# Kernel optimization log

Measured on AMD Instinct MI355X. Metric: run time of the kernel, lower is better.

The kernel has to match this reference:

```python
import jax, jax.numpy as jnp
import numpy as np

N_NODES = 50000
N_EDGES = 800000
D_IN = 64
D_HID = 256
D_OUT = 64


def _linear_params(key, d_in, d_out):
    kw, kb = jax.random.split(key)
    lim = 1.0 / np.sqrt(d_in)
    W = jax.random.uniform(kw, (d_out, d_in), jnp.float32, -lim, lim)
    b = jax.random.uniform(kb, (d_out,), jnp.float32, -lim, lim)
    return W, b


def setup_inputs() -> dict:
    key = jax.random.key(0)
    ks = jax.random.split(key, 10)
    x = jax.random.normal(ks[0], (N_NODES, D_IN), jnp.float32)
    edge_index = jax.random.randint(ks[1], (2, N_EDGES), 0, N_NODES, jnp.int64)
    edge_attr = jax.random.normal(ks[2], (N_EDGES, D_IN), jnp.float32)
    W1m, b1m = _linear_params(ks[3], D_IN, D_HID)
    W1e, b1e = _linear_params(ks[4], D_IN, D_HID)
    W1s, b1s = _linear_params(ks[5], D_IN, D_HID)
    W2m, b2m = _linear_params(ks[6], D_HID, D_OUT)
    W2e, b2e = _linear_params(ks[7], D_IN, D_OUT)
    W2s, b2s = _linear_params(ks[8], D_HID, D_OUT)
    return dict(x=x, edge_index=edge_index, edge_attr=edge_attr,
                W1m=W1m, b1m=b1m, W1e=W1e, b1e=b1e, W1s=W1s, b1s=b1s,
                W2m=W2m, b2m=b2m, W2e=W2e, b2e=b2e, W2s=W2s, b2s=b2s)


def _general_conv(x, src, dst, edge_attr, Wm, bm, We, be, Ws, bs):
    # lin_msg on nodes (cheaper than on edges), then gather to source of each edge
    x_msg = x @ Wm.T + bm                      # [N, d_out]
    edge_term = edge_attr @ We.T + be          # [E, d_out]
    msg = x_msg[src] + edge_term               # [E, d_out]
    agg = jax.ops.segment_sum(msg, dst, num_segments=x.shape[0])  # scatter-add
    return agg + (x @ Ws.T + bs)               # skip connection (in != out channels)


def reference(x, edge_index, edge_attr,
              W1m, b1m, W1e, b1e, W1s, b1s,
              W2m, b2m, W2e, b2e, W2s, b2s):
    src, dst = edge_index[0], edge_index[1]
    h = _general_conv(x, src, dst, edge_attr, W1m, b1m, W1e, b1e, W1s, b1s)
    h = jax.nn.relu(h)  # dropout is identity in eval mode
    out = _general_conv(h, src, dst, edge_attr, W2m, b2m, W2e, b2e, W2s, b2s)
    return jax.nn.relu(out)
```

## Files before the change

kernel.cpp:

```cpp
#include <hip/hip_runtime.h>

#define NN 50000
#define NE 800000
#define SLOTS 64

typedef float f32x4 __attribute__((ext_vector_type(4)));
typedef short short8 __attribute__((ext_vector_type(8)));

static __device__ __forceinline__ unsigned short f2bf(float f){
  unsigned u = __builtin_bit_cast(unsigned, f);
  u = (u + 0x7fffu + ((u >> 16) & 1u)) >> 16;
  return (unsigned short)u;
}
static __device__ __forceinline__ float bf2f(unsigned short b){
  return __builtin_bit_cast(float, ((unsigned)b) << 16);
}

__global__ __launch_bounds__(256) void k_prep(
    const float* __restrict__ x,
    const float* __restrict__ W1m, const float* __restrict__ b1m,
    const float* __restrict__ W1e, const float* __restrict__ b1e,
    const float* __restrict__ W1s, const float* __restrict__ b1s,
    const float* __restrict__ W2m, const float* __restrict__ b2m,
    const float* __restrict__ W2e, const float* __restrict__ b2e,
    const float* __restrict__ W2s, const float* __restrict__ b2s,
    int* __restrict__ cnt,
    unsigned short* __restrict__ xb,
    unsigned short* __restrict__ W1c, unsigned short* __restrict__ W2c,
    unsigned short* __restrict__ W2mb,
    float* __restrict__ b1sA, float* __restrict__ b1dA,
    float* __restrict__ b2sA, float* __restrict__ b2dA)
{
  int g = blockIdx.x*256 + threadIdx.x;
  if (g < NN*8){
    const float4* xp = (const float4*)x;
    float4 v0 = xp[(size_t)g*2], v1 = xp[(size_t)g*2+1];
    short8 o;
    o[0]=(short)f2bf(v0.x); o[1]=(short)f2bf(v0.y); o[2]=(short)f2bf(v0.z); o[3]=(short)f2bf(v0.w);
    o[4]=(short)f2bf(v1.x); o[5]=(short)f2bf(v1.y); o[6]=(short)f2bf(v1.z); o[7]=(short)f2bf(v1.w);
    *(short8*)(xb + (size_t)g*8) = o;
  }
  if (g < NN) cnt[g] = 0;
  if (g < 256*192){
    int oc = g/192, k = g%192;
    float w = (k<64)? W1m[oc*64+k] : (k<128)? W1e[oc*64+(k-64)] : W1s[oc*64+(k-128)];
    W1c[g] = f2bf(w);
  }
  if (g < 64*320){
    int oc = g/320, k = g%320;
    float w = (k<64)? W2e[oc*64+k] : W2s[oc*256+(k-64)];
    W2c[g] = f2bf(w);
  }
  if (g < 64*256){
    W2mb[g] = f2bf(W2m[g]);
  }
  if (g < 256){ b1sA[g] = b1s[g]; b1dA[g] = b1m[g] + b1e[g]; }
  if (g < 64) { b2sA[g] = b2s[g]; b2dA[g] = b2m[g] + b2e[g]; }
}

__global__ __launch_bounds__(256) void k_scatter1(const int* __restrict__ ei, int* __restrict__ cnt,
    int2* __restrict__ pairs_pad){
  int e = (blockIdx.x*256 + threadIdx.x)*4;
  if (e + 4 <= NE){
    int4 s = *(const int4*)(ei + e);
    int4 d = *(const int4*)(ei + NE + e);
    int p0 = atomicAdd(&cnt[d.x], 1); if (p0 < SLOTS) pairs_pad[d.x*SLOTS + p0] = make_int2(s.x, e+0);
    int p1 = atomicAdd(&cnt[d.y], 1); if (p1 < SLOTS) pairs_pad[d.y*SLOTS + p1] = make_int2(s.y, e+1);
    int p2 = atomicAdd(&cnt[d.z], 1); if (p2 < SLOTS) pairs_pad[d.z*SLOTS + p2] = make_int2(s.z, e+2);
    int p3 = atomicAdd(&cnt[d.w], 1); if (p3 < SLOTS) pairs_pad[d.w*SLOTS + p3] = make_int2(s.w, e+3);
  } else {
    for (int q=e; q<NE; q++){
      int s = ei[q], d = ei[NE+q];
      int pos = atomicAdd(&cnt[d], 1);
      if (pos < SLOTS) pairs_pad[d*SLOTS + pos] = make_int2(s, q);
    }
  }
}

__global__ __launch_bounds__(256) void k_aggA(const int2* __restrict__ pairs,
    const int* __restrict__ cnt,
    const unsigned short* __restrict__ xb, const float* __restrict__ ea,
    unsigned short* __restrict__ in1){
  int v = blockIdx.x*4 + (threadIdx.x>>6);
  int lane = threadIdx.x & 63;
  int slot = lane >> 4, fg = lane & 15;
  if (v >= NN) return;
  int beg = v*SLOTS;
  int end = beg + min(cnt[v], SLOTS);
  float xs[4] = {0,0,0,0}, es[4] = {0,0,0,0};
  float xt[4] = {0,0,0,0}, et[4] = {0,0,0,0};
  int i = beg + slot;
  for (; i + 12 < end; i += 16){
    int2 p0 = pairs[i],   p1 = pairs[i+4];
    int2 p2 = pairs[i+8], p3 = pairs[i+12];
    ushort4 xv0 = *(const ushort4*)(xb + (size_t)p0.x*64 + fg*4);
    ushort4 xv1 = *(const ushort4*)(xb + (size_t)p1.x*64 + fg*4);
    ushort4 xv2 = *(const ushort4*)(xb + (size_t)p2.x*64 + fg*4);
    ushort4 xv3 = *(const ushort4*)(xb + (size_t)p3.x*64 + fg*4);
    f32x4 ev0 = __builtin_nontemporal_load((const f32x4*)(ea + (size_t)p0.y*64 + fg*4));
    f32x4 ev1 = __builtin_nontemporal_load((const f32x4*)(ea + (size_t)p1.y*64 + fg*4));
    f32x4 ev2 = __builtin_nontemporal_load((const f32x4*)(ea + (size_t)p2.y*64 + fg*4));
    f32x4 ev3 = __builtin_nontemporal_load((const f32x4*)(ea + (size_t)p3.y*64 + fg*4));
    xs[0]+=bf2f(xv0.x); xs[1]+=bf2f(xv0.y); xs[2]+=bf2f(xv0.z); xs[3]+=bf2f(xv0.w);
    xt[0]+=bf2f(xv1.x); xt[1]+=bf2f(xv1.y); xt[2]+=bf2f(xv1.z); xt[3]+=bf2f(xv1.w);
    xs[0]+=bf2f(xv2.x); xs[1]+=bf2f(xv2.y); xs[2]+=bf2f(xv2.z); xs[3]+=bf2f(xv2.w);
    xt[0]+=bf2f(xv3.x); xt[1]+=bf2f(xv3.y); xt[2]+=bf2f(xv3.z); xt[3]+=bf2f(xv3.w);
    es[0]+=ev0[0]; es[1]+=ev0[1]; es[2]+=ev0[2]; es[3]+=ev0[3];
    et[0]+=ev1[0]; et[1]+=ev1[1]; et[2]+=ev1[2]; et[3]+=ev1[3];
    es[0]+=ev2[0]; es[1]+=ev2[1]; es[2]+=ev2[2]; es[3]+=ev2[3];
    et[0]+=ev3[0]; et[1]+=ev3[1]; et[2]+=ev3[2]; et[3]+=ev3[3];
  }
  for (; i < end; i += 4){
    int2 p0 = pairs[i];
    ushort4 xv0 = *(const ushort4*)(xb + (size_t)p0.x*64 + fg*4);
    f32x4  ev0 = __builtin_nontemporal_load((const f32x4*)(ea + (size_t)p0.y*64 + fg*4));
    xs[0]+=bf2f(xv0.x); xs[1]+=bf2f(xv0.y); xs[2]+=bf2f(xv0.z); xs[3]+=bf2f(xv0.w);
    es[0]+=ev0[0]; es[1]+=ev0[1]; es[2]+=ev0[2]; es[3]+=ev0[3];
  }
  #pragma unroll
  for (int k=0;k<4;k++){
    float a = xs[k] + xt[k];
    float b = es[k] + et[k];
    a += __shfl_xor(a, 16, 64); a += __shfl_xor(a, 32, 64);
    b += __shfl_xor(b, 16, 64); b += __shfl_xor(b, 32, 64);
    xs[k] = a; es[k] = b;
  }
  if (slot == 0){
    unsigned short* o = in1 + (size_t)v*128;
    ushort4 ox; ox.x=f2bf(xs[0]); ox.y=f2bf(xs[1]); ox.z=f2bf(xs[2]); ox.w=f2bf(xs[3]);
    ushort4 oe; oe.x=f2bf(es[0]); oe.y=f2bf(es[1]); oe.z=f2bf(es[2]); oe.w=f2bf(es[3]);
    *(ushort4*)(o + fg*4)      = ox;
    *(ushort4*)(o + 64 + fg*4) = oe;
  }
}

__global__ __launch_bounds__(256) void k_mega(
  const unsigned short* __restrict__ in1, const unsigned short* __restrict__ xb,
  const unsigned short* __restrict__ W1c,
  const unsigned short* __restrict__ W2mb, const unsigned short* __restrict__ W2c,
  const float* __restrict__ b1sA, const float* __restrict__ b1dA,
  const float* __restrict__ b2sA, const float* __restrict__ b2dA,
  const int* __restrict__ cnt,
  unsigned short* __restrict__ y2, float* __restrict__ z)
{
  __shared__ char hl[64*256*2];
  const int tid = threadIdx.x;
  const int w = tid >> 6, l = tid & 63;
  const int lrow = l & 15, lgrp = l >> 4;
  const int n0 = blockIdx.x * 64;
  const int c0 = w * 64;

  f32x4 acc[4][4];
  #pragma unroll
  for (int i=0;i<4;i++)
    #pragma unroll
    for (int j=0;j<4;j++) acc[i][j] = (f32x4)0.f;

  #pragma unroll 2
  for (int ks=0; ks<6; ks++){
    short8 a[4], b[4];
    #pragma unroll
    for (int rf=0; rf<4; rf++){
      int row = n0 + rf*16 + lrow; if (row >= NN) row = NN-1;
      if (ks < 4) a[rf] = *(const short8*)(in1 + (size_t)row*128 + ks*32 + lgrp*8);
      else        a[rf] = *(const short8*)(xb  + (size_t)row*64 + (ks-4)*32 + lgrp*8);
    }
    #pragma unroll
    for (int cf=0; cf<4; cf++){
      b[cf] = *(const short8*)(W1c + (c0 + cf*16 + lrow)*192 + ks*32 + lgrp*8);
    }
    #pragma unroll
    for (int rf=0; rf<4; rf++)
      #pragma unroll
      for (int cf=0; cf<4; cf++)
        acc[rf][cf] = __builtin_amdgcn_mfma_f32_16x16x32_bf16(a[rf], b[cf], acc[rf][cf], 0, 0, 0);
  }

  float dg[4][4];
  #pragma unroll
  for (int rf=0; rf<4; rf++)
    #pragma unroll
    for (int r=0; r<4; r++){
      int node = n0 + rf*16 + 4*lgrp + r;
      dg[rf][r] = (node < NN) ? (float)cnt[node] : 0.f;
    }

  #pragma unroll
  for (int cf=0; cf<4; cf++){
    int oc = c0 + cf*16 + lrow;
    float bs = b1sA[oc], bd = b1dA[oc];
    #pragma unroll
    for (int rf=0; rf<4; rf++){
      #pragma unroll
      for (int r=0; r<4; r++){
        int rloc = rf*16 + 4*lgrp + r;
        float val = acc[rf][cf][r] + bs + dg[rf][r]*bd;
        val = fmaxf(val, 0.f);
        int byte = (rloc*512 + oc*2) ^ ((rloc & 7) << 4);
        *(unsigned short*)(hl + byte) = f2bf(val);
      }
    }
  }
  __syncthreads();

  const int oc2 = w*16 + lrow;
  f32x4 ay[4], az[4];
  #pragma unroll
  for (int i=0;i<4;i++){ ay[i] = (f32x4)0.f; az[i] = (f32x4)0.f; }

  #pragma unroll 2
  for (int ks=0; ks<8; ks++){
    short8 a2[4];
    #pragma unroll
    for (int rf=0; rf<4; rf++){
      int rloc = rf*16 + lrow;
      int byte = (rloc*512 + (ks*32 + lgrp*8)*2) ^ ((rloc & 7) << 4);
      a2[rf] = *(const short8*)(hl + byte);
    }
    short8 by = *(const short8*)(W2mb + oc2*256 + ks*32 + lgrp*8);
    short8 bz = *(const short8*)(W2c  + oc2*320 + 64 + ks*32 + lgrp*8);
    #pragma unroll
    for (int rf=0; rf<4; rf++){
      ay[rf] = __builtin_amdgcn_mfma_f32_16x16x32_bf16(a2[rf], by, ay[rf], 0, 0, 0);
      az[rf] = __builtin_amdgcn_mfma_f32_16x16x32_bf16(a2[rf], bz, az[rf], 0, 0, 0);
    }
  }
  #pragma unroll
  for (int ks=0; ks<2; ks++){
    short8 a3[4];
    #pragma unroll
    for (int rf=0; rf<4; rf++){
      int row = n0 + rf*16 + lrow; if (row >= NN) row = NN-1;
      a3[rf] = *(const short8*)(in1 + (size_t)row*128 + 64 + ks*32 + lgrp*8);
    }
    short8 be = *(const short8*)(W2c + oc2*320 + ks*32 + lgrp*8);
    #pragma unroll
    for (int rf=0; rf<4; rf++)
      az[rf] = __builtin_amdgcn_mfma_f32_16x16x32_bf16(a3[rf], be, az[rf], 0, 0, 0);
  }

  float bs2 = b2sA[oc2], bd2 = b2dA[oc2];
  #pragma unroll
  for (int rf=0; rf<4; rf++){
    #pragma unroll
    for (int r=0; r<4; r++){
      int node = n0 + rf*16 + 4*lgrp + r;
      if (node < NN){
        y2[(size_t)node*64 + oc2] = f2bf(ay[rf][r]);
        z[(size_t)node*64 + oc2]  = az[rf][r] + bs2 + dg[rf][r]*bd2;
      }
    }
  }
}

__global__ __launch_bounds__(256) void k_aggC(const int2* __restrict__ pairs, const int* __restrict__ cnt,
    const unsigned short* __restrict__ y2, const float* __restrict__ z, float* __restrict__ out){
  int v = blockIdx.x*4 + (threadIdx.x>>6);
  int lane = threadIdx.x & 63;
  int slot = lane >> 4, fg = lane & 15;
  if (v >= NN) return;
  int beg = v*SLOTS;
  int end = beg + min(cnt[v], SLOTS);
  float a[4] = {0,0,0,0}, b[4] = {0,0,0,0};
  int i = beg + slot;
  for (; i + 12 < end; i += 16){
    int s0 = pairs[i].x, s1 = pairs[i+4].x, s2 = pairs[i+8].x, s3 = pairs[i+12].x;
    ushort4 y0 = *(const ushort4*)(y2 + (size_t)s0*64 + fg*4);
    ushort4 y1 = *(const ushort4*)(y2 + (size_t)s1*64 + fg*4);
    ushort4 y2v = *(const ushort4*)(y2 + (size_t)s2*64 + fg*4);
    ushort4 y3 = *(const ushort4*)(y2 + (size_t)s3*64 + fg*4);
    a[0]+=bf2f(y0.x); a[1]+=bf2f(y0.y); a[2]+=bf2f(y0.z); a[3]+=bf2f(y0.w);
    b[0]+=bf2f(y1.x); b[1]+=bf2f(y1.y); b[2]+=bf2f(y1.z); b[3]+=bf2f(y1.w);
    a[0]+=bf2f(y2v.x); a[1]+=bf2f(y2v.y); a[2]+=bf2f(y2v.z); a[3]+=bf2f(y2v.w);
    b[0]+=bf2f(y3.x); b[1]+=bf2f(y3.y); b[2]+=bf2f(y3.z); b[3]+=bf2f(y3.w);
  }
  for (; i < end; i += 4){
    int s0 = pairs[i].x;
    ushort4 y0 = *(const ushort4*)(y2 + (size_t)s0*64 + fg*4);
    a[0]+=bf2f(y0.x); a[1]+=bf2f(y0.y); a[2]+=bf2f(y0.z); a[3]+=bf2f(y0.w);
  }
  #pragma unroll
  for (int k=0;k<4;k++){
    float t = a[k] + b[k];
    t += __shfl_xor(t, 16, 64); t += __shfl_xor(t, 32, 64);
    a[k] = t;
  }
  if (slot == 0){
    const float4 zv = *(const float4*)(z + (size_t)v*64 + fg*4);
    f32x4 o;
    o[0] = fmaxf(zv.x + a[0], 0.f);
    o[1] = fmaxf(zv.y + a[1], 0.f);
    o[2] = fmaxf(zv.z + a[2], 0.f);
    o[3] = fmaxf(zv.w + a[3], 0.f);
    __builtin_nontemporal_store(o, (f32x4*)(out + (size_t)v*64 + fg*4));
  }
}

extern "C" void kernel_launch(void* const* d_in, const int* in_sizes, int n_in,
                              void* d_out, int out_size, void* d_ws, size_t ws_size,
                              hipStream_t stream){
  const float* x   = (const float*)d_in[0];
  const int*   ei  = (const int*)d_in[1];
  const float* ea  = (const float*)d_in[2];
  const float* W1m = (const float*)d_in[3];  const float* b1m = (const float*)d_in[4];
  const float* W1e = (const float*)d_in[5];  const float* b1e = (const float*)d_in[6];
  const float* W1s = (const float*)d_in[7];  const float* b1s = (const float*)d_in[8];
  const float* W2m = (const float*)d_in[9];  const float* b2m = (const float*)d_in[10];
  const float* W2e = (const float*)d_in[11]; const float* b2e = (const float*)d_in[12];
  const float* W2s = (const float*)d_in[13]; const float* b2s = (const float*)d_in[14];
  float* out = (float*)d_out;

  char* base = (char*)d_ws;
  size_t off = 0;
  auto alloc = [&](size_t bytes)->void* {
    void* r = base + off;
    off += (bytes + 255) & ~(size_t)255;
    return r;
  };
  int*   cnt       = (int*)  alloc((size_t)NN*4);
  int2*  pairs_pad = (int2*) alloc(((size_t)NN*SLOTS + SLOTS)*8);
  unsigned short* in1 = (unsigned short*)alloc((size_t)NN*128*2);
  unsigned short* y2  = (unsigned short*)alloc((size_t)NN*64*2);
  float*          z   = (float*)         alloc((size_t)NN*64*4);
  unsigned short* xb  = (unsigned short*)alloc((size_t)NN*64*2);
  unsigned short* W1c = (unsigned short*)alloc((size_t)256*192*2);
  unsigned short* W2c = (unsigned short*)alloc((size_t)64*320*2);
  unsigned short* W2mb= (unsigned short*)alloc((size_t)64*256*2);
  float* b1sA = (float*)alloc(256*4);
  float* b1dA = (float*)alloc(256*4);
  float* b2sA = (float*)alloc(64*4);
  float* b2dA = (float*)alloc(64*4);

  k_prep    <<<(NN*8+255)/256, 256, 0, stream>>>(x, W1m,b1m,W1e,b1e,W1s,b1s,
                                               W2m,b2m,W2e,b2e,W2s,b2s,
                                               cnt, xb, W1c, W2c, W2mb,
                                               b1sA,b1dA,b2sA,b2dA);
  k_scatter1<<<(NE/4+255)/256, 256, 0, stream>>>(ei, cnt, pairs_pad);
  k_aggA    <<<(NN+3)/4, 256, 0, stream>>>(pairs_pad, cnt, xb, ea, in1);
  k_mega    <<<(NN+63)/64, 256, 0, stream>>>(in1, xb, W1c, W2mb, W2c,
                                             b1sA, b1dA, b2sA, b2dA, cnt, y2, z);
  k_aggC    <<<(NN+3)/4, 256, 0, stream>>>(pairs_pad, cnt, y2, z, out);
}
```

Before: 186.0 us.

## Split edge pair buffer into SoA arrays and widen aggC gathers to 16 bytes

Replaces the interleaved (src, edge id) int2 buffer with two separate int arrays, so the second aggregation reads only the source indices it needs instead of discarding half of each 8-byte record. k_aggC now uses 8 lanes per neighbour with 16-byte bf16 loads, giving 8 neighbour slots per wavefront and one more shuffle stage in the reduction. The scatter kernel handles 8 edges per thread, and aggA issues its edge-attribute loads before the node-feature gathers. The scatter now does two separate stores per edge instead of one 8-byte store.

```diff
diff --git a/kernel.cpp b/kernel.cpp
--- a/kernel.cpp
+++ b/kernel.cpp
@@ -59,25 +59,32 @@
 }
 
 __global__ __launch_bounds__(256) void k_scatter1(const int* __restrict__ ei, int* __restrict__ cnt,
-    int2* __restrict__ pairs_pad){
-  int e = (blockIdx.x*256 + threadIdx.x)*4;
-  if (e + 4 <= NE){
-    int4 s = *(const int4*)(ei + e);
-    int4 d = *(const int4*)(ei + NE + e);
-    int p0 = atomicAdd(&cnt[d.x], 1); if (p0 < SLOTS) pairs_pad[d.x*SLOTS + p0] = make_int2(s.x, e+0);
-    int p1 = atomicAdd(&cnt[d.y], 1); if (p1 < SLOTS) pairs_pad[d.y*SLOTS + p1] = make_int2(s.y, e+1);
-    int p2 = atomicAdd(&cnt[d.z], 1); if (p2 < SLOTS) pairs_pad[d.z*SLOTS + p2] = make_int2(s.z, e+2);
-    int p3 = atomicAdd(&cnt[d.w], 1); if (p3 < SLOTS) pairs_pad[d.w*SLOTS + p3] = make_int2(s.w, e+3);
+    int* __restrict__ srcs_pad, int* __restrict__ eids_pad){
+  int e = (blockIdx.x*256 + threadIdx.x)*8;
+  if (e + 8 <= NE){
+    int4 s0 = *(const int4*)(ei + e);
+    int4 s1 = *(const int4*)(ei + e + 4);
+    int4 d0 = *(const int4*)(ei + NE + e);
+    int4 d1 = *(const int4*)(ei + NE + e + 4);
+    int p;
+    p = atomicAdd(&cnt[d0.x], 1); if (p < SLOTS){ srcs_pad[d0.x*SLOTS+p]=s0.x; eids_pad[d0.x*SLOTS+p]=e+0; }
+    p = atomicAdd(&cnt[d0.y], 1); if (p < SLOTS){ srcs_pad[d0.y*SLOTS+p]=s0.y; eids_pad[d0.y*SLOTS+p]=e+1; }
+    p = atomicAdd(&cnt[d0.z], 1); if (p < SLOTS){ srcs_pad[d0.z*SLOTS+p]=s0.z; eids_pad[d0.z*SLOTS+p]=e+2; }
+    p = atomicAdd(&cnt[d0.w], 1); if (p < SLOTS){ srcs_pad[d0.w*SLOTS+p]=s0.w; eids_pad[d0.w*SLOTS+p]=e+3; }
+    p = atomicAdd(&cnt[d1.x], 1); if (p < SLOTS){ srcs_pad[d1.x*SLOTS+p]=s1.x; eids_pad[d1.x*SLOTS+p]=e+4; }
+    p = atomicAdd(&cnt[d1.y], 1); if (p < SLOTS){ srcs_pad[d1.y*SLOTS+p]=s1.y; eids_pad[d1.y*SLOTS+p]=e+5; }
+    p = atomicAdd(&cnt[d1.z], 1); if (p < SLOTS){ srcs_pad[d1.z*SLOTS+p]=s1.z; eids_pad[d1.z*SLOTS+p]=e+6; }
+    p = atomicAdd(&cnt[d1.w], 1); if (p < SLOTS){ srcs_pad[d1.w*SLOTS+p]=s1.w; eids_pad[d1.w*SLOTS+p]=e+7; }
   } else {
     for (int q=e; q<NE; q++){
       int s = ei[q], d = ei[NE+q];
       int pos = atomicAdd(&cnt[d], 1);
-      if (pos < SLOTS) pairs_pad[d*SLOTS + pos] = make_int2(s, q);
-    }
-  }
-}
-
-__global__ __launch_bounds__(256) void k_aggA(const int2* __restrict__ pairs,
+      if (pos < SLOTS){ srcs_pad[d*SLOTS+pos] = s; eids_pad[d*SLOTS+pos] = q; }
+    }
+  }
+}
+
+__global__ __launch_bounds__(256) void k_aggA(const int* __restrict__ srcs, const int* __restrict__ eids,
     const int* __restrict__ cnt,
     const unsigned short* __restrict__ xb, const float* __restrict__ ea,
     unsigned short* __restrict__ in1){
@@ -91,31 +98,31 @@
   float xt[4] = {0,0,0,0}, et[4] = {0,0,0,0};
   int i = beg + slot;
   for (; i + 12 < end; i += 16){
-    int2 p0 = pairs[i],   p1 = pairs[i+4];
-    int2 p2 = pairs[i+8], p3 = pairs[i+12];
-    ushort4 xv0 = *(const ushort4*)(xb + (size_t)p0.x*64 + fg*4);
-    ushort4 xv1 = *(const ushort4*)(xb + (size_t)p1.x*64 + fg*4);
-    ushort4 xv2 = *(const ushort4*)(xb + (size_t)p2.x*64 + fg*4);
-    ushort4 xv3 = *(const ushort4*)(xb + (size_t)p3.x*64 + fg*4);
-    f32x4 ev0 = __builtin_nontemporal_load((const f32x4*)(ea + (size_t)p0.y*64 + fg*4));
-    f32x4 ev1 = __builtin_nontemporal_load((const f32x4*)(ea + (size_t)p1.y*64 + fg*4));
-    f32x4 ev2 = __builtin_nontemporal_load((const f32x4*)(ea + (size_t)p2.y*64 + fg*4));
-    f32x4 ev3 = __builtin_nontemporal_load((const f32x4*)(ea + (size_t)p3.y*64 + fg*4));
+    int q0=eids[i], q1=eids[i+4], q2=eids[i+8], q3=eids[i+12];
+    int s0=srcs[i], s1=srcs[i+4], s2=srcs[i+8], s3=srcs[i+12];
+    f32x4 ev0 = __builtin_nontemporal_load((const f32x4*)(ea + (size_t)q0*64 + fg*4));
+    f32x4 ev1 = __builtin_nontemporal_load((const f32x4*)(ea + (size_t)q1*64 + fg*4));
+    f32x4 ev2 = __builtin_nontemporal_load((const f32x4*)(ea + (size_t)q2*64 + fg*4));
+    f32x4 ev3 = __builtin_nontemporal_load((const f32x4*)(ea + (size_t)q3*64 + fg*4));
+    ushort4 xv0 = *(const ushort4*)(xb + (size_t)s0*64 + fg*4);
+    ushort4 xv1 = *(const ushort4*)(xb + (size_t)s1*64 + fg*4);
+    ushort4 xv2 = *(const ushort4*)(xb + (size_t)s2*64 + fg*4);
+    ushort4 xv3 = *(const ushort4*)(xb + (size_t)s3*64 + fg*4);
+    es[0]+=ev0[0]; es[1]+=ev0[1]; es[2]+=ev0[2]; es[3]+=ev0[3];
+    et[0]+=ev1[0]; et[1]+=ev1[1]; et[2]+=ev1[2]; et[3]+=ev1[3];
+    es[0]+=ev2[0]; es[1]+=ev2[1]; es[2]+=ev2[2]; es[3]+=ev2[3];
+    et[0]+=ev3[0]; et[1]+=ev3[1]; et[2]+=ev3[2]; et[3]+=ev3[3];
     xs[0]+=bf2f(xv0.x); xs[1]+=bf2f(xv0.y); xs[2]+=bf2f(xv0.z); xs[3]+=bf2f(xv0.w);
     xt[0]+=bf2f(xv1.x); xt[1]+=bf2f(xv1.y); xt[2]+=bf2f(xv1.z); xt[3]+=bf2f(xv1.w);
     xs[0]+=bf2f(xv2.x); xs[1]+=bf2f(xv2.y); xs[2]+=bf2f(xv2.z); xs[3]+=bf2f(xv2.w);
     xt[0]+=bf2f(xv3.x); xt[1]+=bf2f(xv3.y); xt[2]+=bf2f(xv3.z); xt[3]+=bf2f(xv3.w);
+  }
+  for (; i < end; i += 4){
+    int q0 = eids[i], s0 = srcs[i];
+    f32x4  ev0 = __builtin_nontemporal_load((const f32x4*)(ea + (size_t)q0*64 + fg*4));
+    ushort4 xv0 = *(const ushort4*)(xb + (size_t)s0*64 + fg*4);
     es[0]+=ev0[0]; es[1]+=ev0[1]; es[2]+=ev0[2]; es[3]+=ev0[3];
-    et[0]+=ev1[0]; et[1]+=ev1[1]; et[2]+=ev1[2]; et[3]+=ev1[3];
-    es[0]+=ev2[0]; es[1]+=ev2[1]; es[2]+=ev2[2]; es[3]+=ev2[3];
-    et[0]+=ev3[0]; et[1]+=ev3[1]; et[2]+=ev3[2]; et[3]+=ev3[3];
-  }
-  for (; i < end; i += 4){
-    int2 p0 = pairs[i];
-    ushort4 xv0 = *(const ushort4*)(xb + (size_t)p0.x*64 + fg*4);
-    f32x4  ev0 = __builtin_nontemporal_load((const f32x4*)(ea + (size_t)p0.y*64 + fg*4));
     xs[0]+=bf2f(xv0.x); xs[1]+=bf2f(xv0.y); xs[2]+=bf2f(xv0.z); xs[3]+=bf2f(xv0.w);
-    es[0]+=ev0[0]; es[1]+=ev0[1]; es[2]+=ev0[2]; es[3]+=ev0[3];
   }
   #pragma unroll
   for (int k=0;k<4;k++){
@@ -253,46 +260,45 @@
   }
 }
 
-__global__ __launch_bounds__(256) void k_aggC(const int2* __restrict__ pairs, const int* __restrict__ cnt,
+__global__ __launch_bounds__(256) void k_aggC(const int* __restrict__ srcs, const int* __restrict__ cnt,
     const unsigned short* __restrict__ y2, const float* __restrict__ z, float* __restrict__ out){
   int v = blockIdx.x*4 + (threadIdx.x>>6);
   int lane = threadIdx.x & 63;
-  int slot = lane >> 4, fg = lane & 15;
+  int slot = lane >> 3, fg = lane & 7;
   if (v >= NN) return;
   int beg = v*SLOTS;
   int end = beg + min(cnt[v], SLOTS);
-  float a[4] = {0,0,0,0}, b[4] = {0,0,0,0};
+  float a[8] = {0,0,0,0,0,0,0,0}, b[8] = {0,0,0,0,0,0,0,0};
   int i = beg + slot;
-  for (; i + 12 < end; i += 16){
-    int s0 = pairs[i].x, s1 = pairs[i+4].x, s2 = pairs[i+8].x, s3 = pairs[i+12].x;
-    ushort4 y0 = *(const ushort4*)(y2 + (size_t)s0*64 + fg*4);
-    ushort4 y1 = *(const ushort4*)(y2 + (size_t)s1*64 + fg*4);
-    ushort4 y2v = *(const ushort4*)(y2 + (size_t)s2*64 + fg*4);
-    ushort4 y3 = *(const ushort4*)(y2 + (size_t)s3*64 + fg*4);
-    a[0]+=bf2f(y0.x); a[1]+=bf2f(y0.y); a[2]+=bf2f(y0.z); a[3]+=bf2f(y0.w);
-    b[0]+=bf2f(y1.x); b[1]+=bf2f(y1.y); b[2]+=bf2f(y1.z); b[3]+=bf2f(y1.w);
-    a[0]+=bf2f(y2v.x); a[1]+=bf2f(y2v.y); a[2]+=bf2f(y2v.z); a[3]+=bf2f(y2v.w);
-    b[0]+=bf2f(y3.x); b[1]+=bf2f(y3.y); b[2]+=bf2f(y3.z); b[3]+=bf2f(y3.w);
-  }
-  for (; i < end; i += 4){
-    int s0 = pairs[i].x;
-    ushort4 y0 = *(const ushort4*)(y2 + (size_t)s0*64 + fg*4);
-    a[0]+=bf2f(y0.x); a[1]+=bf2f(y0.y); a[2]+=bf2f(y0.z); a[3]+=bf2f(y0.w);
-  }
-  #pragma unroll
-  for (int k=0;k<4;k++){
+  for (; i + 8 < end; i += 16){
+    int s0 = srcs[i], s1 = srcs[i+8];
+    short8 y0 = *(const short8*)(y2 + (size_t)s0*64 + fg*8);
+    short8 y1 = *(const short8*)(y2 + (size_t)s1*64 + fg*8);
+    #pragma unroll
+    for (int k=0;k<8;k++){ a[k]+=bf2f((unsigned short)y0[k]); b[k]+=bf2f((unsigned short)y1[k]); }
+  }
+  for (; i < end; i += 8){
+    int s0 = srcs[i];
+    short8 y0 = *(const short8*)(y2 + (size_t)s0*64 + fg*8);
+    #pragma unroll
+    for (int k=0;k<8;k++) a[k]+=bf2f((unsigned short)y0[k]);
+  }
+  #pragma unroll
+  for (int k=0;k<8;k++){
     float t = a[k] + b[k];
-    t += __shfl_xor(t, 16, 64); t += __shfl_xor(t, 32, 64);
+    t += __shfl_xor(t, 8, 64); t += __shfl_xor(t, 16, 64); t += __shfl_xor(t, 32, 64);
     a[k] = t;
   }
   if (slot == 0){
-    const float4 zv = *(const float4*)(z + (size_t)v*64 + fg*4);
-    f32x4 o;
-    o[0] = fmaxf(zv.x + a[0], 0.f);
-    o[1] = fmaxf(zv.y + a[1], 0.f);
-    o[2] = fmaxf(zv.z + a[2], 0.f);
-    o[3] = fmaxf(zv.w + a[3], 0.f);
-    __builtin_nontemporal_store(o, (f32x4*)(out + (size_t)v*64 + fg*4));
+    const float4 z0 = *(const float4*)(z + (size_t)v*64 + fg*8);
+    const float4 z1 = *(const float4*)(z + (size_t)v*64 + fg*8 + 4);
+    f32x4 o0, o1;
+    o0[0] = fmaxf(z0.x + a[0], 0.f); o0[1] = fmaxf(z0.y + a[1], 0.f);
+    o0[2] = fmaxf(z0.z + a[2], 0.f); o0[3] = fmaxf(z0.w + a[3], 0.f);
+    o1[0] = fmaxf(z1.x + a[4], 0.f); o1[1] = fmaxf(z1.y + a[5], 0.f);
+    o1[2] = fmaxf(z1.z + a[6], 0.f); o1[3] = fmaxf(z1.w + a[7], 0.f);
+    __builtin_nontemporal_store(o0, (f32x4*)(out + (size_t)v*64 + fg*8));
+    __builtin_nontemporal_store(o1, (f32x4*)(out + (size_t)v*64 + fg*8 + 4));
   }
 }
 
@@ -318,7 +324,8 @@
     return r;
   };
   int*   cnt       = (int*)  alloc((size_t)NN*4);
-  int2*  pairs_pad = (int2*) alloc(((size_t)NN*SLOTS + SLOTS)*8);
+  int*   srcs_pad  = (int*)  alloc(((size_t)NN*SLOTS + SLOTS)*4);
+  int*   eids_pad  = (int*)  alloc(((size_t)NN*SLOTS + SLOTS)*4);
   unsigned short* in1 = (unsigned short*)alloc((size_t)NN*128*2);
   unsigned short* y2  = (unsigned short*)alloc((size_t)NN*64*2);
   float*          z   = (float*)         alloc((size_t)NN*64*4);
@@ -335,9 +342,9 @@
                                                W2m,b2m,W2e,b2e,W2s,b2s,
                                                cnt, xb, W1c, W2c, W2mb,
                                                b1sA,b1dA,b2sA,b2dA);
-  k_scatter1<<<(NE/4+255)/256, 256, 0, stream>>>(ei, cnt, pairs_pad);
-  k_aggA    <<<(NN+3)/4, 256, 0, stream>>>(pairs_pad, cnt, xb, ea, in1);
+  k_scatter1<<<(NE/8+255)/256, 256, 0, stream>>>(ei, cnt, srcs_pad, eids_pad);
+  k_aggA    <<<(NN+3)/4, 256, 0, stream>>>(srcs_pad, eids_pad, cnt, xb, ea, in1);
   k_mega    <<<(NN+63)/64, 256, 0, stream>>>(in1, xb, W1c, W2mb, W2c,
                                              b1sA, b1dA, b2sA, b2dA, cnt, y2, z);
-  k_aggC    <<<(NN+3)/4, 256, 0, stream>>>(pairs_pad, cnt, y2, z, out);
-}
+  k_aggC    <<<(NN+3)/4, 256, 0, stream>>>(srcs_pad, cnt, y2, z, out);
+}
```

New measurement: 193.2 us. 3.9% more time.
